# Optimization experiments

Hardware: AMD Instinct MI355X
Metric: run time of the kernel (lower is better)

## Reference

```python
import jax, jax.numpy as jnp
import numpy as np

B, T, O, D, H = 8, 256, 16, 512, 8
HD = D // H
EPS = 1e-5


def setup_inputs() -> dict:
    key = jax.random.key(0)
    ks = jax.random.split(key, 12)
    s = 1.0 / np.sqrt(D)
    inp = {
        "organ_states": jax.random.normal(ks[0], (B, T, O, D), dtype=jnp.float32),
        "organ_mask": jax.random.randint(ks[1], (B, T, O), 0, 2) > 0,
        "Wq": jax.random.uniform(ks[2], (D, D), jnp.float32, -s, s),
        "bq": jnp.zeros((D,), jnp.float32),
        "Wk": jax.random.uniform(ks[3], (D, D), jnp.float32, -s, s),
        "bk": jnp.zeros((D,), jnp.float32),
        "Wv": jax.random.uniform(ks[4], (D, D), jnp.float32, -s, s),
        "bv": jnp.zeros((D,), jnp.float32),
        "Wo": jax.random.uniform(ks[5], (D, D), jnp.float32, -s, s),
        "bo": jnp.zeros((D,), jnp.float32),
        "gamma": jnp.ones((D,), jnp.float32),
        "beta": jnp.zeros((D,), jnp.float32),
    }
    return inp


def reference(organ_states, organ_mask, Wq, bq, Wk, bk, Wv, bv, Wo, bo, gamma, beta):
    x = organ_states  # (B, T, O, D)
    b, t, o, d = x.shape

    def heads(y):  # (B,T,O,D) -> (B,O,H,T,HD)
        return y.reshape(b, t, o, H, HD).transpose(0, 2, 3, 1, 4)

    q = heads(jnp.einsum('btod,de->btoe', x, Wq) + bq)
    k = heads(jnp.einsum('btod,de->btoe', x, Wk) + bk)
    v = heads(jnp.einsum('btod,de->btoe', x, Wv) + bv)

    scores = jnp.einsum('bohqd,bohkd->bohqk', q, k) / np.sqrt(HD).astype(np.float32)
    # key mask: (B,T,O) -> (B,O,1,1,T)
    mk = organ_mask.transpose(0, 2, 1)[:, :, None, None, :]
    scores = jnp.where(mk, scores, -jnp.inf)
    attn = jax.nn.softmax(scores, axis=-1)
    attn = jnp.where(mk, attn, 0.0)

    att = jnp.einsum('bohqk,bohkd->bohqd', attn, v)  # (B,O,H,T,HD)
    att = att.transpose(0, 3, 1, 2, 4).reshape(b, t, o, d)  # (B,T,O,D)

    out = jnp.einsum('btod,de->btoe', att, Wo) + bo
    res = out + x
    mu = jnp.mean(res, axis=-1, keepdims=True)
    var = jnp.mean(jnp.square(res - mu), axis=-1, keepdims=True)
    y = (res - mu) / jnp.sqrt(var + EPS) * gamma + beta
    y = y * organ_mask[..., None].astype(y.dtype)
    return y
```

## Files before the change

kernel.cpp:

```cpp
#include <hip/hip_runtime.h>


typedef __attribute__((ext_vector_type(8))) short bf16x8;
typedef __attribute__((ext_vector_type(4))) float f32x4;

#define MFMA16(a, b, c) __builtin_amdgcn_mfma_f32_16x16x32_bf16((a), (b), (c), 0, 0, 0)

__device__ __forceinline__ unsigned short f2bf(float f) {
  unsigned int u = __builtin_bit_cast(unsigned int, f);
  u += 0x7fffu + ((u >> 16) & 1u);
  return (unsigned short)(u >> 16);
}

__device__ __forceinline__ unsigned int cvt_pk_bf16(float lo, float hi) {
  unsigned int r;
  asm("v_cvt_pk_bf16_f32 %0, %1, %2" : "=v"(r) : "v"(lo), "v"(hi));
  return r;
}

__device__ __forceinline__ void gload_lds16(const void* g, void* lds) {
  __builtin_amdgcn_global_load_lds((__attribute__((address_space(1))) void*)g,
                                   (__attribute__((address_space(3))) void*)lds,
                                   16, 0, 0);
}

#define WS_ATT  0ull
#define WS_WT   33554432ull
#define WS_Q    35651584ull
#define WS_K    69206016ull
#define WS_V    102760448ull
#define WS_MASK 136314880ull

__global__ void k_prep_w(const float* __restrict__ Wq, const float* __restrict__ Wk,
                         const float* __restrict__ Wv, const float* __restrict__ Wo,
                         unsigned short* __restrict__ Wt) {
  __shared__ float tl[64][65];
  const float* src = blockIdx.z == 0 ? Wq : blockIdx.z == 1 ? Wk : blockIdx.z == 2 ? Wv : Wo;
  const int d0 = blockIdx.x * 64, e0 = blockIdx.y * 64;
  const int tid = threadIdx.x;
  {
    const int dr = tid >> 2, ec = (tid & 3) * 16;
    const float4* srow = (const float4*)(src + (size_t)(d0 + dr) * 512 + e0 + ec);
#pragma unroll
    for (int j = 0; j < 4; ++j) {
      float4 v = srow[j];
      tl[dr][ec + j * 4 + 0] = v.x;
      tl[dr][ec + j * 4 + 1] = v.y;
      tl[dr][ec + j * 4 + 2] = v.z;
      tl[dr][ec + j * 4 + 3] = v.w;
    }
  }
  __syncthreads();
  const int dd0 = (tid & 7) * 8;
#pragma unroll
  for (int i = 0; i < 2; ++i) {
    int e = i * 32 + (tid >> 3);
    bf16x8 ob;
#pragma unroll
    for (int j = 0; j < 8; ++j) ob[j] = (short)f2bf(tl[dd0 + j][e]);
    *(bf16x8*)(Wt + ((size_t)blockIdx.z * 512 + e0 + e) * 512 + d0 + dd0) = ob;
  }
}

__global__ void k_prep_mask(const void* __restrict__ mraw, unsigned char* __restrict__ mout) {
  const unsigned int* u = (const unsigned int*)mraw;
  int lane = threadIdx.x & 63;
  int packed = __any(u[lane] > 1u);
  int idx = blockIdx.x * 256 + threadIdx.x;
  unsigned char m;
  if (packed) m = ((const unsigned char*)mraw)[idx] ? 1 : 0;
  else        m = u[idx] ? 1 : 0;
  mout[idx] = m;
}

__global__ __launch_bounds__(256) void k_qkv(
    const float* __restrict__ X, const unsigned short* __restrict__ Wt,
    const float* __restrict__ bq, const float* __restrict__ bk, const float* __restrict__ bv,
    unsigned short* __restrict__ Qb, unsigned short* __restrict__ Kb, unsigned short* __restrict__ Vb) {
  __shared__ char sm[32768];
  const int tid = threadIdx.x, l = tid & 63, w = tid >> 6;
  const int lane15 = l & 15, quad = l >> 4;
  const int flat = blockIdx.x;
  const int swz = (flat & 7) * 384 + (flat >> 3);
  const int mtile = swz & 255, yb = swz >> 8;
  const int which = yb >> 2, ntile = yb & 3;
  const int rbase = mtile * 128;
  const unsigned short* wgp = Wt + ((size_t)which * 512 + ntile * 128) * 512;
  const int wr = w >> 1, wc = w & 1;
  const int srow = tid >> 3;
  const int c16 = (tid & 7) * 16;
  char* const abase = sm;
  char* const bbase = sm + 16384;
  f32x4 acc[4][4] = {};
  for (int ks = 0; ks < 8; ++ks) {
    __syncthreads();
#pragma unroll
    for (int i = 0; i < 4; ++i) {
      int row = i * 32 + srow;
      gload_lds16((const char*)wgp + (size_t)row * 1024 + ks * 128 + (c16 ^ ((row & 7) << 4)),
                  bbase + i * 4096 + w * 1024);
    }
#pragma unroll
    for (int i = 0; i < 4; ++i) {
      int row = i * 32 + srow;
      const float4* xs = (const float4*)(X + (size_t)(rbase + row) * 512 + ks * 64 + (tid & 7) * 8);
      float4 v0 = xs[0], v1 = xs[1];
      uint4 pk;
      pk.x = cvt_pk_bf16(v0.x, v0.y);
      pk.y = cvt_pk_bf16(v0.z, v0.w);
      pk.z = cvt_pk_bf16(v1.x, v1.y);
      pk.w = cvt_pk_bf16(v1.z, v1.w);
      *(uint4*)(abase + row * 128 + (c16 ^ ((row & 7) << 4))) = pk;
    }
    __syncthreads();
#pragma unroll
    for (int kc = 0; kc < 2; ++kc) {
      bf16x8 af[4], bfr[4];
#pragma unroll
      for (int mt = 0; mt < 4; ++mt) {
        int row = wr * 64 + mt * 16 + lane15;
        af[mt] = *(const bf16x8*)(abase + row * 128 + ((kc * 64 + quad * 16) ^ ((row & 7) << 4)));
      }
#pragma unroll
      for (int nt = 0; nt < 4; ++nt) {
        int col = wc * 64 + nt * 16 + lane15;
        bfr[nt] = *(const bf16x8*)(bbase + col * 128 + ((kc * 64 + quad * 16) ^ ((col & 7) << 4)));
      }
#pragma unroll
      for (int mt = 0; mt < 4; ++mt)
#pragma unroll
        for (int nt = 0; nt < 4; ++nt)
          acc[mt][nt] = MFMA16(af[mt], bfr[nt], acc[mt][nt]);
    }
  }
  const float* bias = (which == 0) ? bq : (which == 1) ? bk : bv;
  unsigned short* dst = (which == 0) ? Qb : (which == 1) ? Kb : Vb;
  const int h = ntile * 2 + wc;
#pragma unroll
  for (int mt = 0; mt < 4; ++mt) {
#pragma unroll
    for (int reg = 0; reg < 4; ++reg) {
      int r = rbase + wr * 64 + mt * 16 + quad * 4 + reg;
      int b = r >> 12, t = (r >> 4) & 255, o = r & 15;
      size_t base_bt = (size_t)((b * 16 + o) * 8 + h) * 16384 + (size_t)t * 64;
#pragma unroll
      for (int nt = 0; nt < 4; ++nt) {
        int hd = nt * 16 + lane15;
        dst[base_bt + hd] = f2bf(acc[mt][nt][reg] + bias[h * 64 + hd]);
      }
    }
  }
}

__global__ __launch_bounds__(512, 2) void k_attn(
    const unsigned short* __restrict__ Qb, const unsigned short* __restrict__ Kb,
    const unsigned short* __restrict__ Vb, const unsigned char* __restrict__ Mc,
    unsigned short* __restrict__ att) {
  __shared__ char sm[99328];
  const int tid = threadIdx.x, l = tid & 63, w = tid >> 6;
  const int lane15 = l & 15, quad = l >> 4;
  const int bid = blockIdx.x;
  const int h = bid & 7, o = (bid >> 3) & 15, b = bid >> 7;
  const size_t head = (size_t)((b * 16 + o) * 8 + h) * 16384;
  const unsigned short* qh = Qb + head;
  const char* kg = (const char*)(Kb + head);
  const unsigned short* vh = Vb + head;

  {
    const int srow = tid >> 3;
    const int c16 = (tid & 7) * 16;
    char* kdst = sm + w * 1024;
#pragma unroll
    for (int i = 0; i < 4; ++i) {
      int t = i * 64 + srow;
      gload_lds16(kg + (size_t)t * 128 + (c16 ^ ((t & 7) << 4)), kdst + i * 8192);
    }
  }
  const int q0 = w * 32;
  bf16x8 qf[2][2];
#pragma unroll
  for (int mt = 0; mt < 2; ++mt)
#pragma unroll
    for (int kc = 0; kc < 2; ++kc)
      qf[mt][kc] = *(const bf16x8*)(qh + (size_t)(q0 + mt * 16 + lane15) * 64 + kc * 32 + quad * 8);
  unsigned short vreg[32];
  {
    const int hd = tid & 63, tq = tid >> 6;
#pragma unroll
    for (int i = 0; i < 4; ++i)
#pragma unroll
      for (int j = 0; j < 8; ++j)
        vreg[i * 8 + j] = vh[(size_t)(tq * 32 + i * 8 + j) * 64 + hd];
  }
  float* maskb = (float*)(sm + 98304);
  if (tid < 256)
    maskb[tid] = Mc[(size_t)(b * 256 + tid) * 16 + o] ? 0.0f : -43280.0f;
  {
    const int hd = tid & 63, tq = tid >> 6;
    const int rowb = 32768 + hd * 512;
    const int swz = (hd & 7) << 4;
#pragma unroll
    for (int i = 0; i < 4; ++i) {
      bf16x8 pk;
#pragma unroll
      for (int j = 0; j < 8; ++j) pk[j] = (short)vreg[i * 8 + j];
      int t0 = tq * 32 + i * 8;
      *(bf16x8*)(sm + rowb + ((t0 * 2) ^ swz)) = pk;
    }
  }
  __syncthreads();

  f32x4 sacc[2][16] = {};
#pragma unroll
  for (int c = 0; c < 4; ++c) {
#pragma unroll
    for (int kc = 0; kc < 2; ++kc) {
      bf16x8 kf[4];
#pragma unroll
      for (int nt = 0; nt < 4; ++nt) {
        int t = c * 64 + nt * 16 + lane15;
        int byt = t * 128 + ((kc * 64 + quad * 16) ^ ((t & 7) << 4));
        kf[nt] = *(const bf16x8*)(sm + byt);
      }
#pragma unroll
      for (int mt = 0; mt < 2; ++mt)
#pragma unroll
        for (int nt = 0; nt < 4; ++nt)
          sacc[mt][c * 4 + nt] = MFMA16(qf[mt][kc], kf[nt], sacc[mt][c * 4 + nt]);
    }
  }

  float biasv[16];
#pragma unroll
  for (int g = 0; g < 16; ++g) biasv[g] = maskb[g * 16 + lane15];
  float inv[2][4];
#pragma unroll
  for (int mt = 0; mt < 2; ++mt) {
#pragma unroll
    for (int reg = 0; reg < 4; ++reg) {
      float v[16];
#pragma unroll
      for (int g = 0; g < 16; ++g)
        v[g] = sacc[mt][g][reg] * 0.18033688f + biasv[g];
      float m = v[0];
#pragma unroll
      for (int g = 1; g < 16; ++g) m = fmaxf(m, v[g]);
#pragma unroll
      for (int d = 1; d < 16; d <<= 1) m = fmaxf(m, __shfl_xor(m, d));
      float rs = 0.f;
#pragma unroll
      for (int g = 0; g < 16; ++g) {
        float p = __builtin_amdgcn_exp2f(v[g] - m);
        sacc[mt][g][reg] = p;
        rs += p;
      }
#pragma unroll
      for (int d = 1; d < 16; d <<= 1) rs += __shfl_xor(rs, d);
      inv[mt][reg] = 1.0f / rs;
    }
  }

  char* pb = sm + 65536 + w * 4096;
  f32x4 pv[2][4] = {};
#pragma unroll
  for (int c = 0; c < 4; ++c) {
#pragma unroll
    for (int mt = 0; mt < 2; ++mt)
#pragma unroll
      for (int nt = 0; nt < 4; ++nt)
#pragma unroll
        for (int reg = 0; reg < 4; ++reg) {
          int qrow = mt * 16 + quad * 4 + reg;
          int byt = (qrow * 128 + (nt * 16 + lane15) * 2) ^ ((qrow & 7) << 4);
          *(unsigned short*)(pb + byt) = f2bf(sacc[mt][c * 4 + nt][reg]);
        }
#pragma unroll
    for (int kc = 0; kc < 2; ++kc) {
      bf16x8 pa[2], vbr[4];
#pragma unroll
      for (int mt = 0; mt < 2; ++mt) {
        int qrow = mt * 16 + lane15;
        int byt = (qrow * 128 + kc * 64 + quad * 16) ^ ((qrow & 7) << 4);
        pa[mt] = *(const bf16x8*)(pb + byt);
      }
#pragma unroll
      for (int nh = 0; nh < 4; ++nh) {
        int hd = nh * 16 + lane15;
        int byt = hd * 512 + ((c * 128 + kc * 64 + quad * 16) ^ ((hd & 7) << 4));
        vbr[nh] = *(const bf16x8*)(sm + 32768 + byt);
      }
#pragma unroll
      for (int mt = 0; mt < 2; ++mt)
#pragma unroll
        for (int nh = 0; nh < 4; ++nh)
          pv[mt][nh] = MFMA16(pa[mt], vbr[nh], pv[mt][nh]);
    }
  }

#pragma unroll
  for (int mt = 0; mt < 2; ++mt) {
#pragma unroll
    for (int reg = 0; reg < 4; ++reg) {
      int q = q0 + mt * 16 + quad * 4 + reg;
      size_t r = (size_t)(b * 256 + q) * 16 + o;
      float iv = inv[mt][reg];
#pragma unroll
      for (int nh = 0; nh < 4; ++nh)
        att[r * 512 + h * 64 + nh * 16 + lane15] = f2bf(pv[mt][nh][reg] * iv);
    }
  }
}

__global__ __launch_bounds__(512) void k_oproj(
    const unsigned short* __restrict__ A, const unsigned short* __restrict__ Wt,
    const float* __restrict__ bo, const float* __restrict__ X,
    const unsigned char* __restrict__ Mc, const float* __restrict__ gamma,
    const float* __restrict__ beta, float* __restrict__ out) {
  __shared__ char sm[73728];
  __shared__ float psum[64][8];
  __shared__ float psumsq[64][8];
  __shared__ float smean[64];
  __shared__ float srstd[64];
  const int tid = threadIdx.x, l = tid & 63, w = tid >> 6;
  const int lane15 = l & 15, quad = l >> 4;
  const int rbase = blockIdx.x * 64;
  const char* ag = (const char*)A;
  const char* wgp = (const char*)(Wt + (size_t)1536 * 512);
  const int srow = tid >> 3;
  const int c16 = (tid & 7) * 16;
  const int swz_a = c16 ^ ((srow & 7) << 4);
  char* adst = sm + w * 1024;
  f32x4 acc[4][4] = {};
  for (int ks = 0; ks < 8; ++ks) {
    __syncthreads();
    gload_lds16(ag + (size_t)(rbase + srow) * 1024 + ks * 128 + swz_a, adst);
#pragma unroll
    for (int p = 0; p < 8; ++p) {
      int er = p * 64 + srow;
      gload_lds16(wgp + (size_t)er * 1024 + ks * 128 + (c16 ^ ((er & 7) << 4)),
                  sm + 8192 + p * 8192 + w * 1024);
    }
    __syncthreads();
#pragma unroll
    for (int kc = 0; kc < 2; ++kc) {
      bf16x8 af[4], bfr[4];
#pragma unroll
      for (int mt = 0; mt < 4; ++mt) {
        int row = mt * 16 + lane15;
        int byt = (row * 128 + kc * 64 + quad * 16) ^ ((row & 7) << 4);
        af[mt] = *(const bf16x8*)(sm + byt);
      }
#pragma unroll
      for (int nt = 0; nt < 4; ++nt) {
        int col = w * 64 + nt * 16 + lane15;
        int byt = (col * 128 + kc * 64 + quad * 16) ^ ((col & 7) << 4);
        bfr[nt] = *(const bf16x8*)(sm + 8192 + byt);
      }
#pragma unroll
      for (int mt = 0; mt < 4; ++mt)
#pragma unroll
        for (int nt = 0; nt < 4; ++nt)
          acc[mt][nt] = MFMA16(af[mt], bfr[nt], acc[mt][nt]);
    }
  }
#pragma unroll
  for (int mt = 0; mt < 4; ++mt) {
#pragma unroll
    for (int reg = 0; reg < 4; ++reg) {
      int rl = mt * 16 + quad * 4 + reg;
      int r = rbase + rl;
      float s1 = 0.f, s2 = 0.f;
#pragma unroll
      for (int nt = 0; nt < 4; ++nt) {
        int col = w * 64 + nt * 16 + lane15;
        float v = acc[mt][nt][reg] + bo[col] + X[(size_t)r * 512 + col];
        acc[mt][nt][reg] = v;
        s1 += v; s2 += v * v;
      }
#pragma unroll
      for (int d = 1; d < 16; d <<= 1) { s1 += __shfl_xor(s1, d); s2 += __shfl_xor(s2, d); }
      if (lane15 == 0) { psum[rl][w] = s1; psumsq[rl][w] = s2; }
    }
  }
  __syncthreads();
  if (tid < 64) {
    float a = 0.f, q = 0.f;
#pragma unroll
    for (int j = 0; j < 8; ++j) { a += psum[tid][j]; q += psumsq[tid][j]; }
    float mu = a * (1.f / 512.f);
    float var = q * (1.f / 512.f) - mu * mu;
    smean[tid] = mu;
    srstd[tid] = rsqrtf(fmaxf(var, 0.f) + 1e-5f);
  }
  __syncthreads();
#pragma unroll
  for (int mt = 0; mt < 4; ++mt) {
#pragma unroll
    for (int reg = 0; reg < 4; ++reg) {
      int rl = mt * 16 + quad * 4 + reg;
      int r = rbase + rl;
      float mu = smean[rl], rs = srstd[rl];
      float mkf = Mc[r] ? 1.f : 0.f;
#pragma unroll
      for (int nt = 0; nt < 4; ++nt) {
        int col = w * 64 + nt * 16 + lane15;
        float y = (acc[mt][nt][reg] - mu) * rs * gamma[col] + beta[col];
        out[(size_t)r * 512 + col] = y * mkf;
      }
    }
  }
}

extern "C" void kernel_launch(void* const* d_in, const int* in_sizes, int n_in,
                              void* d_out, int out_size, void* d_ws, size_t ws_size,
                              hipStream_t stream) {
  const float* X     = (const float*)d_in[0];
  const void*  Mraw  = d_in[1];
  const float* Wq    = (const float*)d_in[2];
  const float* bq    = (const float*)d_in[3];
  const float* Wk    = (const float*)d_in[4];
  const float* bk    = (const float*)d_in[5];
  const float* Wv    = (const float*)d_in[6];
  const float* bv    = (const float*)d_in[7];
  const float* Wo    = (const float*)d_in[8];
  const float* bo    = (const float*)d_in[9];
  const float* gamma = (const float*)d_in[10];
  const float* beta  = (const float*)d_in[11];

  char* ws = (char*)d_ws;
  unsigned short* att = (unsigned short*)(ws + WS_ATT);
  unsigned short* Wt  = (unsigned short*)(ws + WS_WT);
  unsigned short* Qb  = (unsigned short*)(ws + WS_Q);
  unsigned short* Kb  = (unsigned short*)(ws + WS_K);
  unsigned short* Vb  = (unsigned short*)(ws + WS_V);
  unsigned char*  Mc  = (unsigned char*)(ws + WS_MASK);

  hipLaunchKernelGGL(k_prep_w,   dim3(8, 8, 4), dim3(256), 0, stream, Wq, Wk, Wv, Wo, Wt);
  hipLaunchKernelGGL(k_prep_mask,dim3(128),     dim3(256), 0, stream, Mraw, Mc);
  hipLaunchKernelGGL(k_qkv,      dim3(3072),    dim3(256), 0, stream, X, Wt, bq, bk, bv, Qb, Kb, Vb);
  hipLaunchKernelGGL(k_attn,     dim3(1024),    dim3(512), 0, stream, Qb, Kb, Vb, Mc, att);
  hipLaunchKernelGGL(k_oproj,    dim3(512),     dim3(512), 0, stream, att, Wt, bo, X, Mc, gamma, beta,
                     (float*)d_out);
}
```

Before: 328.7 us.

## Pre-convert X to bf16 and load QKV A-tiles via direct global-to-LDS

Adds a separate kernel that converts the fp32 activations to bf16 once, into the workspace region also reused later for the attention output. The QKV GEMM then stages both operands with async global_load_lds instead of register loads plus in-kernel conversion. Previously each of the 12 column tiles re-read and re-converted fp32 X. The block-index swizzle is also replaced by a plain row-major tile mapping, which changes L2 reuse. The cost is an extra pass over X (read 64MB, write 32MB) and one more launch.

```diff
diff --git a/kernel.cpp b/kernel.cpp
--- a/kernel.cpp
+++ b/kernel.cpp
@@ -12,24 +12,26 @@
   return (unsigned short)(u >> 16);
 }
 
-__device__ __forceinline__ unsigned int cvt_pk_bf16(float lo, float hi) {
-  unsigned int r;
-  asm("v_cvt_pk_bf16_f32 %0, %1, %2" : "=v"(r) : "v"(lo), "v"(hi));
-  return r;
-}
-
 __device__ __forceinline__ void gload_lds16(const void* g, void* lds) {
   __builtin_amdgcn_global_load_lds((__attribute__((address_space(1))) void*)g,
                                    (__attribute__((address_space(3))) void*)lds,
                                    16, 0, 0);
 }
 
-#define WS_ATT  0ull
+#define WS_XB   0ull
 #define WS_WT   33554432ull
 #define WS_Q    35651584ull
 #define WS_K    69206016ull
 #define WS_V    102760448ull
 #define WS_MASK 136314880ull
+
+__global__ void k_cvt_x(const float* __restrict__ x, unsigned short* __restrict__ xb) {
+  int i = blockIdx.x * 256 + threadIdx.x;
+  float4 v = ((const float4*)x)[i];
+  ushort4 o;
+  o.x = f2bf(v.x); o.y = f2bf(v.y); o.z = f2bf(v.z); o.w = f2bf(v.w);
+  ((ushort4*)xb)[i] = o;
+}
 
 __global__ void k_prep_w(const float* __restrict__ Wq, const float* __restrict__ Wk,
                          const float* __restrict__ Wv, const float* __restrict__ Wo,
@@ -74,18 +76,18 @@
 }
 
 __global__ __launch_bounds__(256) void k_qkv(
-    const float* __restrict__ X, const unsigned short* __restrict__ Wt,
+    const unsigned short* __restrict__ Xb, const unsigned short* __restrict__ Wt,
     const float* __restrict__ bq, const float* __restrict__ bk, const float* __restrict__ bv,
     unsigned short* __restrict__ Qb, unsigned short* __restrict__ Kb, unsigned short* __restrict__ Vb) {
   __shared__ char sm[32768];
   const int tid = threadIdx.x, l = tid & 63, w = tid >> 6;
   const int lane15 = l & 15, quad = l >> 4;
   const int flat = blockIdx.x;
-  const int swz = (flat & 7) * 384 + (flat >> 3);
-  const int mtile = swz & 255, yb = swz >> 8;
+  const int mtile = flat / 12, yb = flat % 12;
   const int which = yb >> 2, ntile = yb & 3;
   const int rbase = mtile * 128;
-  const unsigned short* wgp = Wt + ((size_t)which * 512 + ntile * 128) * 512;
+  const char* xg = (const char*)Xb + (size_t)rbase * 1024;
+  const char* wgp = (const char*)(Wt + ((size_t)which * 512 + ntile * 128) * 512);
   const int wr = w >> 1, wc = w & 1;
   const int srow = tid >> 3;
   const int c16 = (tid & 7) * 16;
@@ -97,20 +99,9 @@
 #pragma unroll
     for (int i = 0; i < 4; ++i) {
       int row = i * 32 + srow;
-      gload_lds16((const char*)wgp + (size_t)row * 1024 + ks * 128 + (c16 ^ ((row & 7) << 4)),
-                  bbase + i * 4096 + w * 1024);
-    }
-#pragma unroll
-    for (int i = 0; i < 4; ++i) {
-      int row = i * 32 + srow;
-      const float4* xs = (const float4*)(X + (size_t)(rbase + row) * 512 + ks * 64 + (tid & 7) * 8);
-      float4 v0 = xs[0], v1 = xs[1];
-      uint4 pk;
-      pk.x = cvt_pk_bf16(v0.x, v0.y);
-      pk.y = cvt_pk_bf16(v0.z, v0.w);
-      pk.z = cvt_pk_bf16(v1.x, v1.y);
-      pk.w = cvt_pk_bf16(v1.z, v1.w);
-      *(uint4*)(abase + row * 128 + (c16 ^ ((row & 7) << 4))) = pk;
+      int swz = c16 ^ ((row & 7) << 4);
+      gload_lds16(xg + (size_t)row * 1024 + ks * 128 + swz, abase + i * 4096 + w * 1024);
+      gload_lds16(wgp + (size_t)row * 1024 + ks * 128 + swz, bbase + i * 4096 + w * 1024);
     }
     __syncthreads();
 #pragma unroll
@@ -428,16 +419,18 @@
   const float* beta  = (const float*)d_in[11];
 
   char* ws = (char*)d_ws;
-  unsigned short* att = (unsigned short*)(ws + WS_ATT);
+  unsigned short* Xb  = (unsigned short*)(ws + WS_XB);
   unsigned short* Wt  = (unsigned short*)(ws + WS_WT);
   unsigned short* Qb  = (unsigned short*)(ws + WS_Q);
   unsigned short* Kb  = (unsigned short*)(ws + WS_K);
   unsigned short* Vb  = (unsigned short*)(ws + WS_V);
   unsigned char*  Mc  = (unsigned char*)(ws + WS_MASK);
-
+  unsigned short* att = Xb;
+
+  hipLaunchKernelGGL(k_cvt_x,    dim3(16384),   dim3(256), 0, stream, X, Xb);
   hipLaunchKernelGGL(k_prep_w,   dim3(8, 8, 4), dim3(256), 0, stream, Wq, Wk, Wv, Wo, Wt);
   hipLaunchKernelGGL(k_prep_mask,dim3(128),     dim3(256), 0, stream, Mraw, Mc);
-  hipLaunchKernelGGL(k_qkv,      dim3(3072),    dim3(256), 0, stream, X, Wt, bq, bk, bv, Qb, Kb, Vb);
+  hipLaunchKernelGGL(k_qkv,      dim3(3072),    dim3(256), 0, stream, Xb, Wt, bq, bk, bv, Qb, Kb, Vb);
   hipLaunchKernelGGL(k_attn,     dim3(1024),    dim3(512), 0, stream, Qb, Kb, Vb, Mc, att);
   hipLaunchKernelGGL(k_oproj,    dim3(512),     dim3(512), 0, stream, att, Wt, bo, X, Mc, gamma, beta,
                      (float*)d_out);
```

Measured after the change: 297.5 us. 1.1x faster.
